# Optimization experiments

Hardware: AMD Instinct MI355X
Metric: run time of the kernel (lower is better)

The kernel has to match this reference:

```python
import jax, jax.numpy as jnp
import numpy as np
import math

B, S, H, D = 4, 2048, 16, 64
HID = H * D  # 1024


def setup_inputs() -> dict:
    key = jax.random.key(0)
    ks = jax.random.split(key, 9)
    s_in = 1.0 / math.sqrt(D)
    s_hid = 1.0 / math.sqrt(HID)
    return {
        "x": jax.random.normal(ks[0], (B, S, D), dtype=jnp.float32),
        "Wq": jax.random.uniform(ks[1], (D, HID), jnp.float32, -s_in, s_in),
        "bq": jax.random.uniform(ks[2], (HID,), jnp.float32, -s_in, s_in),
        "Wk": jax.random.uniform(ks[3], (D, HID), jnp.float32, -s_in, s_in),
        "bk": jax.random.uniform(ks[4], (HID,), jnp.float32, -s_in, s_in),
        "Wv": jax.random.uniform(ks[5], (D, HID), jnp.float32, -s_in, s_in),
        "bv": jax.random.uniform(ks[6], (HID,), jnp.float32, -s_in, s_in),
        "Wo": jax.random.uniform(ks[7], (HID, D), jnp.float32, -s_hid, s_hid),
        "bo": jax.random.uniform(ks[8], (D,), jnp.float32, -s_hid, s_hid),
    }


def reference(x, Wq, bq, Wk, bk, Wv, bv, Wo, bo):
    b, s, _ = x.shape
    # projections: [B,S,D] -> [B,S,HID] -> [B,H,S,D]
    q = (x @ Wq + bq).reshape(b, s, H, D).transpose(0, 2, 1, 3)
    k = (x @ Wk + bk).reshape(b, s, H, D).transpose(0, 2, 1, 3)
    v = (x @ Wv + bv).reshape(b, s, H, D).transpose(0, 2, 1, 3)
    scores = jnp.einsum("bhqd,bhkd->bhqk", q, k) / math.sqrt(D)
    # causal mask: -inf strictly above the diagonal
    causal = jnp.tril(jnp.ones((s, s), dtype=bool))
    scores = jnp.where(causal, scores, -jnp.inf)
    attn = jax.nn.softmax(scores, axis=-1)  # dropout is identity at eval
    out = jnp.einsum("bhqk,bhkd->bhqd", attn, v)
    out = out.transpose(0, 2, 1, 3).reshape(b, s, HID)
    return out @ Wo + bo  # [B,S,D]
```

## Files before the change

### kernel.cpp

```cpp
#include <hip/hip_runtime.h>
#include <hip/hip_bf16.h>

#define B 4
#define S 2048
#define H 16
#define D 64
#define HID 1024

typedef __hip_bfloat16 bf16;
typedef __attribute__((ext_vector_type(8))) short bf16x8;
typedef __attribute__((ext_vector_type(4))) short bf16x4;
typedef __attribute__((ext_vector_type(4))) float f32x4;

static __device__ __forceinline__ float b2f(bf16 v) { return __bfloat162float(v); }

static __device__ __forceinline__ unsigned pkbf(float a, float b) {
    union { bf16 h; unsigned short u; } ua, ub;
    ua.h = __float2bfloat16(a);
    ub.h = __float2bfloat16(b);
    return (unsigned)ua.u | ((unsigned)ub.u << 16);
}

#define SCL 0.18033688011112042f

#define QSTR 72
#define VTS  132

__global__ __launch_bounds__(256) void qkv_mfma_kernel(
    const float* __restrict__ x,
    const float* __restrict__ Wq, const float* __restrict__ bq,
    const float* __restrict__ Wk, const float* __restrict__ bk,
    const float* __restrict__ Wv, const float* __restrict__ bv,
    bf16* __restrict__ q, bf16* __restrict__ k, bf16* __restrict__ v)
{
    __shared__ __align__(16) char smem[36864];
    __shared__ float bs[128];
    bf16* Xs = (bf16*)smem;
    bf16* Wt = (bf16*)(smem + 128 * QSTR * 2);

    const int tid = threadIdx.x;
    const int mat = blockIdx.y >> 3;
    const int N0  = (blockIdx.y & 7) * 128;
    const int m0  = blockIdx.x * 128;

    const float* W    = (mat == 0) ? Wq : (mat == 1) ? Wk : Wv;
    const float* bias = (mat == 0) ? bq : (mat == 1) ? bk : bv;
    bf16*        dst  = (mat == 0) ? q  : (mat == 1) ? k  : v;
    const float  oscale = (mat == 0) ? SCL : 1.0f;

    #pragma unroll
    for (int i = 0; i < 8; ++i) {
        int item = i * 256 + tid;
        int row = item >> 4, f4 = item & 15;
        float4 xv = *(const float4*)&x[(size_t)(m0 + row) * D + f4 * 4];
        union { bf16 h[4]; bf16x4 v4; } u;
        u.h[0] = __float2bfloat16(xv.x); u.h[1] = __float2bfloat16(xv.y);
        u.h[2] = __float2bfloat16(xv.z); u.h[3] = __float2bfloat16(xv.w);
        *(bf16x4*)&Xs[row * QSTR + f4 * 4] = u.v4;
    }
    #pragma unroll
    for (int i = 0; i < 2; ++i) {
        int unit = i * 256 + tid;
        int n0 = (unit & 31) * 4, k0 = (unit >> 5) * 4;
        float wv[4][4];
        #pragma unroll
        for (int j = 0; j < 4; ++j) {
            float4 t = *(const float4*)&W[(size_t)(k0 + j) * HID + N0 + n0];
            wv[j][0] = t.x; wv[j][1] = t.y; wv[j][2] = t.z; wv[j][3] = t.w;
        }
        #pragma unroll
        for (int dn = 0; dn < 4; ++dn) {
            union { bf16 h[4]; bf16x4 v4; } u;
            #pragma unroll
            for (int j = 0; j < 4; ++j) u.h[j] = __float2bfloat16(wv[j][dn]);
            *(bf16x4*)&Wt[(n0 + dn) * QSTR + k0] = u.v4;
        }
    }
    if (tid < 128) bs[tid] = bias[N0 + tid];
    __syncthreads();

    const int lane = tid & 63, wave = tid >> 6;
    const int c = lane & 15, quad = lane >> 4;

    bf16x8 af[2][2];
    #pragma unroll
    for (int mg = 0; mg < 2; ++mg)
        #pragma unroll
        for (int kc = 0; kc < 2; ++kc)
            af[mg][kc] = *(const bf16x8*)&Xs[(wave * 32 + mg * 16 + c) * QSTR + kc * 32 + quad * 8];

    f32x4 acc[2][8];
    #pragma unroll
    for (int mg = 0; mg < 2; ++mg)
        #pragma unroll
        for (int ng = 0; ng < 8; ++ng)
            acc[mg][ng] = (f32x4){0.f, 0.f, 0.f, 0.f};

    if (mat == 2) {
        #pragma unroll
        for (int ng = 0; ng < 8; ++ng) {
            bf16x8 bf0 = *(const bf16x8*)&Wt[(ng * 16 + c) * QSTR + quad * 8];
            bf16x8 bf1 = *(const bf16x8*)&Wt[(ng * 16 + c) * QSTR + 32 + quad * 8];
            #pragma unroll
            for (int mg = 0; mg < 2; ++mg) {
                acc[mg][ng] = __builtin_amdgcn_mfma_f32_16x16x32_bf16(af[mg][0], bf0, acc[mg][ng], 0, 0, 0);
                acc[mg][ng] = __builtin_amdgcn_mfma_f32_16x16x32_bf16(af[mg][1], bf1, acc[mg][ng], 0, 0, 0);
            }
        }
    } else {
        #pragma unroll
        for (int ng = 0; ng < 8; ++ng) {
            bf16x8 bf0 = *(const bf16x8*)&Wt[(ng * 16 + c) * QSTR + quad * 8];
            bf16x8 bf1 = *(const bf16x8*)&Wt[(ng * 16 + c) * QSTR + 32 + quad * 8];
            #pragma unroll
            for (int mg = 0; mg < 2; ++mg) {
                acc[mg][ng] = __builtin_amdgcn_mfma_f32_16x16x32_bf16(bf0, af[mg][0], acc[mg][ng], 0, 0, 0);
                acc[mg][ng] = __builtin_amdgcn_mfma_f32_16x16x32_bf16(bf1, af[mg][1], acc[mg][ng], 0, 0, 0);
            }
        }
    }

    if (mat == 2) {
        bf16* T = (bf16*)smem;
        __syncthreads();
        #pragma unroll
        for (int ng = 0; ng < 8; ++ng) {
            int hid_l = ng * 16 + c;
            float bb_ = bs[hid_l];
            #pragma unroll
            for (int mg = 0; mg < 2; ++mg) {
                int ss_l = wave * 32 + mg * 16 + quad * 4;
                union { bf16 h4[4]; bf16x4 v4; } u;
                #pragma unroll
                for (int r = 0; r < 4; ++r)
                    u.h4[r] = __float2bfloat16(acc[mg][ng][r] + bb_);
                *(bf16x4*)&T[hid_l * VTS + ss_l] = u.v4;
            }
        }
        __syncthreads();
        const int b_ = m0 >> 11, ss0 = m0 & (S - 1);
        #pragma unroll
        for (int pass = 0; pass < 8; ++pass) {
            int unit = pass * 256 + tid;
            int dd_l = unit >> 4, u8 = unit & 15;
            bf16x8 val = *(const bf16x8*)&T[dd_l * VTS + u8 * 8];
            int h = (N0 >> 6) + (dd_l >> 6), ddg = dd_l & 63;
            *(bf16x8*)&dst[((size_t)(b_ * H + h) * D + ddg) * S + ss0 + u8 * 8] = val;
        }
    } else {
        bf16* T2 = (bf16*)smem;
        __syncthreads();
        #pragma unroll
        for (int ng = 0; ng < 8; ++ng) {
            float4 bb4 = *(const float4*)&bs[ng * 16 + quad * 4];
            #pragma unroll
            for (int mg = 0; mg < 2; ++mg) {
                int mrow = wave * 32 + mg * 16 + c;
                union { bf16 h4[4]; bf16x4 v4; } u;
                #pragma unroll
                for (int r = 0; r < 4; ++r)
                    u.h4[r] = __float2bfloat16((acc[mg][ng][r] + (&bb4.x)[r]) * oscale);
                *(bf16x4*)&T2[mrow * VTS + ng * 16 + quad * 4] = u.v4;
            }
        }
        __syncthreads();
        const int b_ = m0 >> 11, ss0 = m0 & (S - 1);
        #pragma unroll
        for (int pass = 0; pass < 8; ++pass) {
            int unit = pass * 256 + tid;
            int row_l = unit >> 4, n8 = unit & 15;
            bf16x8 val = *(const bf16x8*)&T2[row_l * VTS + n8 * 8];
            int n_g = N0 + n8 * 8;
            int h = n_g >> 6, dd = n_g & 63;
            *(bf16x8*)&dst[((size_t)(b_ * H + h) * S + ss0 + row_l) * D + dd] = val;
        }
    }
}

#define BT   64
#define NT   (S / BT)

__global__ __launch_bounds__(256) void flash_mfma_kernel(
    const bf16* __restrict__ qg, const bf16* __restrict__ kg,
    const bf16* __restrict__ vg, bf16* __restrict__ og)
{
    __shared__ bf16 Ks[2][BT * 64];
    __shared__ bf16 Vt[2][BT * 64];
    __shared__ bf16 Ps[4][16 * 64];

    const int tid  = threadIdx.x;
    const int wave = tid >> 6;
    const int lane = tid & 63;
    const int c    = lane & 15;
    const int quad = lane >> 4;

    const int L    = (int)blockIdx.x + 16 * (int)blockIdx.y;
    const int xcd  = L & 7;
    const int slot = L >> 3;
    const int pair = slot & 15;
    const int bh   = xcd * 8 + (slot >> 4);
    const int b_   = bh >> 4, h_ = bh & 15;
    const size_t hbase = (size_t)bh * S * D;
    bf16* myP = &Ps[wave][0];
    const int srow = wave * 16 + c;

    const int qta = pair;
    const int qtb = NT - 1 - pair;

    const int sr0 = tid >> 3, g0 = tid & 7;
    const int sr1 = sr0 + 32;
    const int sc0 = g0 * 8;
    const int so0 = sr0 * 64 + ((g0 ^ (sr0 & 7)) << 3);
    const int so1 = sr1 * 64 + ((g0 ^ (sr1 & 7)) << 3);
    const int cx7 = c & 7;

    bf16x8 qfa0, qfa1, qfb0, qfb1;
    {
        const size_t ra = hbase + (size_t)(qta * BT + srow) * D;
        const size_t rb = hbase + (size_t)(qtb * BT + srow) * D;
        qfa0 = *(const bf16x8*)(qg + ra + quad * 8);
        qfa1 = *(const bf16x8*)(qg + ra + 32 + quad * 8);
        qfb0 = *(const bf16x8*)(qg + rb + quad * 8);
        qfb1 = *(const bf16x8*)(qg + rb + 32 + quad * 8);
    }

    float la = 0.f, lb = 0.f;
    f32x4 ota[4], otb[4];
    #pragma unroll
    for (int jn = 0; jn < 4; ++jn) {
        ota[jn] = (f32x4){0.f, 0.f, 0.f, 0.f};
        otb[jn] = (f32x4){0.f, 0.f, 0.f, 0.f};
    }

    auto front = [&](const bf16* Kb, bf16x8 qf0, bf16x8 qf1, float& l1, bool diag) {
        f32x4 st[4];
        #pragma unroll
        for (int jn = 0; jn < 4; ++jn) {
            const int rb_ = (jn * 16 + c) * 64;
            bf16x8 kf0 = *(const bf16x8*)&Kb[rb_ + ((quad       ^ cx7) << 3)];
            bf16x8 kf1 = *(const bf16x8*)&Kb[rb_ + (((quad + 4) ^ cx7) << 3)];
            f32x4 s = {0.f, 0.f, 0.f, 0.f};
            s = __builtin_amdgcn_mfma_f32_16x16x32_bf16(kf0, qf0, s, 0, 0, 0);
            s = __builtin_amdgcn_mfma_f32_16x16x32_bf16(kf1, qf1, s, 0, 0, 0);
            st[jn] = s;
        }
        #pragma unroll
        for (int jn = 0; jn < 4; ++jn) {
            float p0 = __builtin_amdgcn_exp2f(st[jn][0]);
            float p1 = __builtin_amdgcn_exp2f(st[jn][1]);
            float p2 = __builtin_amdgcn_exp2f(st[jn][2]);
            float p3 = __builtin_amdgcn_exp2f(st[jn][3]);
            if (diag) {
                int col = jn * 16 + quad * 4;
                if (col     > srow) p0 = 0.f;
                if (col + 1 > srow) p1 = 0.f;
                if (col + 2 > srow) p2 = 0.f;
                if (col + 3 > srow) p3 = 0.f;
            }
            l1 += (p0 + p1) + (p2 + p3);
            union { unsigned w[2]; bf16x4 v4; } pk;
            pk.w[0] = pkbf(p0, p1);
            pk.w[1] = pkbf(p2, p3);
            *(bf16x4*)&myP[c * 64 + (((2 * jn + (quad >> 1)) ^ cx7) << 3) + (quad & 1) * 4] = pk.v4;
        }
    };
    auto pv = [&](const bf16* Vb, f32x4* ot) {
        #pragma unroll
        for (int kc = 0; kc < 2; ++kc) {
            bf16x8 pf = *(const bf16x8*)&myP[c * 64 + (((kc * 4 + quad) ^ cx7) << 3)];
            #pragma unroll
            for (int jn = 0; jn < 4; ++jn) {
                const int rb_ = (jn * 16 + c) * 64;
                bf16x8 vf = *(const bf16x8*)&Vb[rb_ + (((kc * 4 + quad) ^ cx7) << 3)];
                ot[jn] = __builtin_amdgcn_mfma_f32_16x16x32_bf16(vf, pf, ot[jn], 0, 0, 0);
            }
        }
    };

    bf16x8 kreg0, kreg1, vreg0, vreg1;
    kreg0 = *(const bf16x8*)(kg + hbase + (size_t)sr0 * D + sc0);
    kreg1 = *(const bf16x8*)(kg + hbase + (size_t)sr1 * D + sc0);
    vreg0 = *(const bf16x8*)(vg + hbase + (size_t)sr0 * S + sc0);
    vreg1 = *(const bf16x8*)(vg + hbase + (size_t)sr1 * S + sc0);
    *(bf16x8*)&Ks[0][so0] = kreg0;
    *(bf16x8*)&Ks[0][so1] = kreg1;
    *(bf16x8*)&Vt[0][so0] = vreg0;
    *(bf16x8*)&Vt[0][so1] = vreg1;
    {
        const int nb = BT;
        kreg0 = *(const bf16x8*)(kg + hbase + (size_t)(nb + sr0) * D + sc0);
        kreg1 = *(const bf16x8*)(kg + hbase + (size_t)(nb + sr1) * D + sc0);
        vreg0 = *(const bf16x8*)(vg + hbase + (size_t)sr0 * S + nb + sc0);
        vreg1 = *(const bf16x8*)(vg + hbase + (size_t)sr1 * S + nb + sc0);
    }
    __syncthreads();

    int cur = 0;
    for (int kt = 0; kt <= qtb; ++kt) {
        if (kt < qtb) {
            *(bf16x8*)&Ks[cur ^ 1][so0] = kreg0;
            *(bf16x8*)&Ks[cur ^ 1][so1] = kreg1;
            *(bf16x8*)&Vt[cur ^ 1][so0] = vreg0;
            *(bf16x8*)&Vt[cur ^ 1][so1] = vreg1;
            if (kt + 1 < qtb) {
                const int nb = (kt + 2) * BT;
                kreg0 = *(const bf16x8*)(kg + hbase + (size_t)(nb + sr0) * D + sc0);
                kreg1 = *(const bf16x8*)(kg + hbase + (size_t)(nb + sr1) * D + sc0);
                vreg0 = *(const bf16x8*)(vg + hbase + (size_t)sr0 * S + nb + sc0);
                vreg1 = *(const bf16x8*)(vg + hbase + (size_t)sr1 * S + nb + sc0);
            }
        }

        const bf16* Kb = &Ks[cur][0];
        const bf16* Vb = &Vt[cur][0];
        front(Kb, qfb0, qfb1, lb, kt == qtb);
        pv(Vb, otb);
        if (kt <= qta) {
            front(Kb, qfa0, qfa1, la, kt == qta);
            pv(Vb, ota);
        }

        if (kt < qtb) {
            __syncthreads();
            cur ^= 1;
        }
    }

    {
        float lt = lb;
        lt += __shfl_xor(lt, 16);
        lt += __shfl_xor(lt, 32);
        const float inv = 1.f / lt;
        const size_t obase = ((size_t)(b_ * S + qtb * BT + srow)) * HID + h_ * 64 + quad * 4;
        #pragma unroll
        for (int jn = 0; jn < 4; ++jn) {
            union { bf16 h4[4]; bf16x4 v4; } u;
            #pragma unroll
            for (int r = 0; r < 4; ++r)
                u.h4[r] = __float2bfloat16(otb[jn][r] * inv);
            *(bf16x4*)&og[obase + jn * 16] = u.v4;
        }
    }
    {
        float lt = la;
        lt += __shfl_xor(lt, 16);
        lt += __shfl_xor(lt, 32);
        const float inv = 1.f / lt;
        const size_t obase = ((size_t)(b_ * S + qta * BT + srow)) * HID + h_ * 64 + quad * 4;
        #pragma unroll
        for (int jn = 0; jn < 4; ++jn) {
            union { bf16 h4[4]; bf16x4 v4; } u;
            #pragma unroll
            for (int r = 0; r < 4; ++r)
                u.h4[r] = __float2bfloat16(ota[jn][r] * inv);
            *(bf16x4*)&og[obase + jn * 16] = u.v4;
        }
    }
}

__global__ __launch_bounds__(256) void out_proj_mfma_kernel(
    const bf16* __restrict__ o, const float* __restrict__ Wo,
    const float* __restrict__ bo, float* __restrict__ out)
{
    __shared__ bf16 Os[32 * QSTR];
    __shared__ bf16 Wot[64 * QSTR];
    __shared__ float bos[64];

    const int tid = threadIdx.x;
    const int m0  = blockIdx.x * 32;
    const int lane = tid & 63, wave = tid >> 6;
    const int c = lane & 15, quad = lane >> 4;
    const int mtile = wave >> 1;
    const int ngb   = (wave & 1) * 2;

    const int orow = tid >> 3, ooct = tid & 7;
    const int n0 = (tid & 15) * 4, kk0 = (tid >> 4) * 4;

    if (tid < 64) bos[tid] = bo[tid];

    bf16x8 oreg = *(const bf16x8*)(o + (size_t)(m0 + orow) * HID + ooct * 8);
    float4 w4[4];
    #pragma unroll
    for (int j = 0; j < 4; ++j)
        w4[j] = *(const float4*)&Wo[(size_t)(kk0 + j) * 64 + n0];

    f32x4 acc[2];
    acc[0] = (f32x4){0.f, 0.f, 0.f, 0.f};
    acc[1] = (f32x4){0.f, 0.f, 0.f, 0.f};

    for (int chunk = 0; chunk < 16; ++chunk) {
        __syncthreads();
        *(bf16x8*)&Os[orow * QSTR + ooct * 8] = oreg;
        #pragma unroll
        for (int dn = 0; dn < 4; ++dn) {
            union { bf16 h[4]; bf16x4 v4; } u;
            u.h[0] = __float2bfloat16((&w4[0].x)[dn]);
            u.h[1] = __float2bfloat16((&w4[1].x)[dn]);
            u.h[2] = __float2bfloat16((&w4[2].x)[dn]);
            u.h[3] = __float2bfloat16((&w4[3].x)[dn]);
            *(bf16x4*)&Wot[(n0 + dn) * QSTR + kk0] = u.v4;
        }
        __syncthreads();

        if (chunk < 15) {
            const int k1 = (chunk + 1) * 64;
            oreg = *(const bf16x8*)(o + (size_t)(m0 + orow) * HID + k1 + ooct * 8);
            #pragma unroll
            for (int j = 0; j < 4; ++j)
                w4[j] = *(const float4*)&Wo[(size_t)(k1 + kk0 + j) * 64 + n0];
        }

        bf16x8 a0 = *(const bf16x8*)&Os[(mtile * 16 + c) * QSTR + quad * 8];
        bf16x8 a1 = *(const bf16x8*)&Os[(mtile * 16 + c) * QSTR + 32 + quad * 8];
        #pragma unroll
        for (int g = 0; g < 2; ++g) {
            int ng = ngb + g;
            bf16x8 b0 = *(const bf16x8*)&Wot[(ng * 16 + c) * QSTR + quad * 8];
            bf16x8 b1 = *(const bf16x8*)&Wot[(ng * 16 + c) * QSTR + 32 + quad * 8];
            acc[g] = __builtin_amdgcn_mfma_f32_16x16x32_bf16(a0, b0, acc[g], 0, 0, 0);
            acc[g] = __builtin_amdgcn_mfma_f32_16x16x32_bf16(a1, b1, acc[g], 0, 0, 0);
        }
    }

    #pragma unroll
    for (int g = 0; g < 2; ++g) {
        int n = (ngb + g) * 16 + c;
        float bb_ = bos[n];
        #pragma unroll
        for (int r = 0; r < 4; ++r) {
            int row = m0 + mtile * 16 + quad * 4 + r;
            out[(size_t)row * 64 + n] = acc[g][r] + bb_;
        }
    }
}

extern "C" void kernel_launch(void* const* d_in, const int* in_sizes, int n_in,
                              void* d_out, int out_size, void* d_ws, size_t ws_size,
                              hipStream_t stream)
{
    const float* x  = (const float*)d_in[0];
    const float* Wq = (const float*)d_in[1];
    const float* bq = (const float*)d_in[2];
    const float* Wk = (const float*)d_in[3];
    const float* bk = (const float*)d_in[4];
    const float* Wv = (const float*)d_in[5];
    const float* bv = (const float*)d_in[6];
    const float* Wo = (const float*)d_in[7];
    const float* bo = (const float*)d_in[8];

    char* ws = (char*)d_ws;
    const size_t qkv_bytes = (size_t)B * S * HID * sizeof(bf16);
    bf16* qw = (bf16*)(ws);
    bf16* kw = (bf16*)(ws + qkv_bytes);
    bf16* vw = (bf16*)(ws + 2 * qkv_bytes);
    bf16* ow = (bf16*)(ws + 3 * qkv_bytes);

    qkv_mfma_kernel<<<dim3(B * S / 128, 24), 256, 0, stream>>>(
        x, Wq, bq, Wk, bk, Wv, bv, qw, kw, vw);

    flash_mfma_kernel<<<dim3(NT / 2, B * H), 256, 0, stream>>>(qw, kw, vw, ow);

    out_proj_mfma_kernel<<<dim3(B * S / 32), 256, 0, stream>>>(ow, Wo, bo,
                                                               (float*)d_out);
}
```

Before: 162.9 us.

## Fuse Q/K/V projections into one block loop reusing x fragments in registers

The QKV kernel now launches 8 column blocks instead of 24, and each block loops over the three weight matrices. The x tile is loaded once straight from global memory into MFMA A-fragments in registers, with no LDS staging, and reused for Q, K and V. This cuts redundant x loads and conversions but gives a third as many blocks with longer serial work each. The flash kernel also gains explicit lgkmcnt waits between the P writes and the PV reads, and packs P through a uint2 store.

```diff
diff --git a/kernel.cpp b/kernel.cpp
--- a/kernel.cpp
+++ b/kernel.cpp
@@ -35,144 +35,145 @@
 {
     __shared__ __align__(16) char smem[36864];
     __shared__ float bs[128];
-    bf16* Xs = (bf16*)smem;
-    bf16* Wt = (bf16*)(smem + 128 * QSTR * 2);
+    bf16* Wt = (bf16*)smem;
 
     const int tid = threadIdx.x;
-    const int mat = blockIdx.y >> 3;
-    const int N0  = (blockIdx.y & 7) * 128;
+    const int N0  = blockIdx.y * 128;
     const int m0  = blockIdx.x * 128;
-
-    const float* W    = (mat == 0) ? Wq : (mat == 1) ? Wk : Wv;
-    const float* bias = (mat == 0) ? bq : (mat == 1) ? bk : bv;
-    bf16*        dst  = (mat == 0) ? q  : (mat == 1) ? k  : v;
-    const float  oscale = (mat == 0) ? SCL : 1.0f;
-
-    #pragma unroll
-    for (int i = 0; i < 8; ++i) {
-        int item = i * 256 + tid;
-        int row = item >> 4, f4 = item & 15;
-        float4 xv = *(const float4*)&x[(size_t)(m0 + row) * D + f4 * 4];
-        union { bf16 h[4]; bf16x4 v4; } u;
-        u.h[0] = __float2bfloat16(xv.x); u.h[1] = __float2bfloat16(xv.y);
-        u.h[2] = __float2bfloat16(xv.z); u.h[3] = __float2bfloat16(xv.w);
-        *(bf16x4*)&Xs[row * QSTR + f4 * 4] = u.v4;
-    }
-    #pragma unroll
-    for (int i = 0; i < 2; ++i) {
-        int unit = i * 256 + tid;
-        int n0 = (unit & 31) * 4, k0 = (unit >> 5) * 4;
-        float wv[4][4];
-        #pragma unroll
-        for (int j = 0; j < 4; ++j) {
-            float4 t = *(const float4*)&W[(size_t)(k0 + j) * HID + N0 + n0];
-            wv[j][0] = t.x; wv[j][1] = t.y; wv[j][2] = t.z; wv[j][3] = t.w;
-        }
-        #pragma unroll
-        for (int dn = 0; dn < 4; ++dn) {
-            union { bf16 h[4]; bf16x4 v4; } u;
-            #pragma unroll
-            for (int j = 0; j < 4; ++j) u.h[j] = __float2bfloat16(wv[j][dn]);
-            *(bf16x4*)&Wt[(n0 + dn) * QSTR + k0] = u.v4;
-        }
-    }
-    if (tid < 128) bs[tid] = bias[N0 + tid];
-    __syncthreads();
 
     const int lane = tid & 63, wave = tid >> 6;
     const int c = lane & 15, quad = lane >> 4;
 
     bf16x8 af[2][2];
     #pragma unroll
-    for (int mg = 0; mg < 2; ++mg)
-        #pragma unroll
-        for (int kc = 0; kc < 2; ++kc)
-            af[mg][kc] = *(const bf16x8*)&Xs[(wave * 32 + mg * 16 + c) * QSTR + kc * 32 + quad * 8];
-
-    f32x4 acc[2][8];
-    #pragma unroll
-    for (int mg = 0; mg < 2; ++mg)
-        #pragma unroll
-        for (int ng = 0; ng < 8; ++ng)
-            acc[mg][ng] = (f32x4){0.f, 0.f, 0.f, 0.f};
-
-    if (mat == 2) {
-        #pragma unroll
-        for (int ng = 0; ng < 8; ++ng) {
-            bf16x8 bf0 = *(const bf16x8*)&Wt[(ng * 16 + c) * QSTR + quad * 8];
-            bf16x8 bf1 = *(const bf16x8*)&Wt[(ng * 16 + c) * QSTR + 32 + quad * 8];
-            #pragma unroll
-            for (int mg = 0; mg < 2; ++mg) {
-                acc[mg][ng] = __builtin_amdgcn_mfma_f32_16x16x32_bf16(af[mg][0], bf0, acc[mg][ng], 0, 0, 0);
-                acc[mg][ng] = __builtin_amdgcn_mfma_f32_16x16x32_bf16(af[mg][1], bf1, acc[mg][ng], 0, 0, 0);
-            }
-        }
-    } else {
-        #pragma unroll
-        for (int ng = 0; ng < 8; ++ng) {
-            bf16x8 bf0 = *(const bf16x8*)&Wt[(ng * 16 + c) * QSTR + quad * 8];
-            bf16x8 bf1 = *(const bf16x8*)&Wt[(ng * 16 + c) * QSTR + 32 + quad * 8];
-            #pragma unroll
-            for (int mg = 0; mg < 2; ++mg) {
-                acc[mg][ng] = __builtin_amdgcn_mfma_f32_16x16x32_bf16(bf0, af[mg][0], acc[mg][ng], 0, 0, 0);
-                acc[mg][ng] = __builtin_amdgcn_mfma_f32_16x16x32_bf16(bf1, af[mg][1], acc[mg][ng], 0, 0, 0);
-            }
-        }
-    }
-
-    if (mat == 2) {
-        bf16* T = (bf16*)smem;
+    for (int mg = 0; mg < 2; ++mg) {
+        const float* xr = &x[(size_t)(m0 + wave * 32 + mg * 16 + c) * D];
+        #pragma unroll
+        for (int kc = 0; kc < 2; ++kc) {
+            float4 lo = *(const float4*)&xr[kc * 32 + quad * 8];
+            float4 hi = *(const float4*)&xr[kc * 32 + quad * 8 + 4];
+            union { bf16 h[8]; bf16x8 v8; } u;
+            u.h[0] = __float2bfloat16(lo.x); u.h[1] = __float2bfloat16(lo.y);
+            u.h[2] = __float2bfloat16(lo.z); u.h[3] = __float2bfloat16(lo.w);
+            u.h[4] = __float2bfloat16(hi.x); u.h[5] = __float2bfloat16(hi.y);
+            u.h[6] = __float2bfloat16(hi.z); u.h[7] = __float2bfloat16(hi.w);
+            af[mg][kc] = u.v8;
+        }
+    }
+
+    const int b_ = m0 >> 11, ss0 = m0 & (S - 1);
+
+    for (int mat = 0; mat < 3; ++mat) {
+        const float* W    = (mat == 0) ? Wq : (mat == 1) ? Wk : Wv;
+        const float* bias = (mat == 0) ? bq : (mat == 1) ? bk : bv;
+        bf16*        dst  = (mat == 0) ? q  : (mat == 1) ? k  : v;
+        const float  oscale = (mat == 0) ? SCL : 1.0f;
+
         __syncthreads();
         #pragma unroll
-        for (int ng = 0; ng < 8; ++ng) {
-            int hid_l = ng * 16 + c;
-            float bb_ = bs[hid_l];
-            #pragma unroll
-            for (int mg = 0; mg < 2; ++mg) {
-                int ss_l = wave * 32 + mg * 16 + quad * 4;
-                union { bf16 h4[4]; bf16x4 v4; } u;
+        for (int i = 0; i < 2; ++i) {
+            int unit = i * 256 + tid;
+            int n0 = (unit & 31) * 4, k0 = (unit >> 5) * 4;
+            float wv[4][4];
+            #pragma unroll
+            for (int j = 0; j < 4; ++j) {
+                float4 t = *(const float4*)&W[(size_t)(k0 + j) * HID + N0 + n0];
+                wv[j][0] = t.x; wv[j][1] = t.y; wv[j][2] = t.z; wv[j][3] = t.w;
+            }
+            #pragma unroll
+            for (int dn = 0; dn < 4; ++dn) {
+                union { bf16 h[4]; bf16x4 v4; } u;
                 #pragma unroll
-                for (int r = 0; r < 4; ++r)
-                    u.h4[r] = __float2bfloat16(acc[mg][ng][r] + bb_);
-                *(bf16x4*)&T[hid_l * VTS + ss_l] = u.v4;
-            }
-        }
+                for (int j = 0; j < 4; ++j) u.h[j] = __float2bfloat16(wv[j][dn]);
+                *(bf16x4*)&Wt[(n0 + dn) * QSTR + k0] = u.v4;
+            }
+        }
+        if (tid < 128) bs[tid] = bias[N0 + tid];
         __syncthreads();
-        const int b_ = m0 >> 11, ss0 = m0 & (S - 1);
-        #pragma unroll
-        for (int pass = 0; pass < 8; ++pass) {
-            int unit = pass * 256 + tid;
-            int dd_l = unit >> 4, u8 = unit & 15;
-            bf16x8 val = *(const bf16x8*)&T[dd_l * VTS + u8 * 8];
-            int h = (N0 >> 6) + (dd_l >> 6), ddg = dd_l & 63;
-            *(bf16x8*)&dst[((size_t)(b_ * H + h) * D + ddg) * S + ss0 + u8 * 8] = val;
-        }
-    } else {
-        bf16* T2 = (bf16*)smem;
+
+        f32x4 acc[2][8];
+        #pragma unroll
+        for (int mg = 0; mg < 2; ++mg)
+            #pragma unroll
+            for (int ng = 0; ng < 8; ++ng)
+                acc[mg][ng] = (f32x4){0.f, 0.f, 0.f, 0.f};
+
+        if (mat == 2) {
+            #pragma unroll
+            for (int ng = 0; ng < 8; ++ng) {
+                bf16x8 bf0 = *(const bf16x8*)&Wt[(ng * 16 + c) * QSTR + quad * 8];
+                bf16x8 bf1 = *(const bf16x8*)&Wt[(ng * 16 + c) * QSTR + 32 + quad * 8];
+                #pragma unroll
+                for (int mg = 0; mg < 2; ++mg) {
+                    acc[mg][ng] = __builtin_amdgcn_mfma_f32_16x16x32_bf16(af[mg][0], bf0, acc[mg][ng], 0, 0, 0);
+                    acc[mg][ng] = __builtin_amdgcn_mfma_f32_16x16x32_bf16(af[mg][1], bf1, acc[mg][ng], 0, 0, 0);
+                }
+            }
+        } else {
+            #pragma unroll
+            for (int ng = 0; ng < 8; ++ng) {
+                bf16x8 bf0 = *(const bf16x8*)&Wt[(ng * 16 + c) * QSTR + quad * 8];
+                bf16x8 bf1 = *(const bf16x8*)&Wt[(ng * 16 + c) * QSTR + 32 + quad * 8];
+                #pragma unroll
+                for (int mg = 0; mg < 2; ++mg) {
+                    acc[mg][ng] = __builtin_amdgcn_mfma_f32_16x16x32_bf16(bf0, af[mg][0], acc[mg][ng], 0, 0, 0);
+                    acc[mg][ng] = __builtin_amdgcn_mfma_f32_16x16x32_bf16(bf1, af[mg][1], acc[mg][ng], 0, 0, 0);
+                }
+            }
+        }
+
         __syncthreads();
-        #pragma unroll
-        for (int ng = 0; ng < 8; ++ng) {
-            float4 bb4 = *(const float4*)&bs[ng * 16 + quad * 4];
-            #pragma unroll
-            for (int mg = 0; mg < 2; ++mg) {
-                int mrow = wave * 32 + mg * 16 + c;
-                union { bf16 h4[4]; bf16x4 v4; } u;
+
+        if (mat == 2) {
+            bf16* T = (bf16*)smem;
+            #pragma unroll
+            for (int ng = 0; ng < 8; ++ng) {
+                int hid_l = ng * 16 + c;
+                float bb_ = bs[hid_l];
                 #pragma unroll
-                for (int r = 0; r < 4; ++r)
-                    u.h4[r] = __float2bfloat16((acc[mg][ng][r] + (&bb4.x)[r]) * oscale);
-                *(bf16x4*)&T2[mrow * VTS + ng * 16 + quad * 4] = u.v4;
-            }
-        }
-        __syncthreads();
-        const int b_ = m0 >> 11, ss0 = m0 & (S - 1);
-        #pragma unroll
-        for (int pass = 0; pass < 8; ++pass) {
-            int unit = pass * 256 + tid;
-            int row_l = unit >> 4, n8 = unit & 15;
-            bf16x8 val = *(const bf16x8*)&T2[row_l * VTS + n8 * 8];
-            int n_g = N0 + n8 * 8;
-            int h = n_g >> 6, dd = n_g & 63;
-            *(bf16x8*)&dst[((size_t)(b_ * H + h) * S + ss0 + row_l) * D + dd] = val;
+                for (int mg = 0; mg < 2; ++mg) {
+                    int ss_l = wave * 32 + mg * 16 + quad * 4;
+                    union { bf16 h4[4]; bf16x4 v4; } u;
+                    #pragma unroll
+                    for (int r = 0; r < 4; ++r)
+                        u.h4[r] = __float2bfloat16(acc[mg][ng][r] + bb_);
+                    *(bf16x4*)&T[hid_l * VTS + ss_l] = u.v4;
+                }
+            }
+            __syncthreads();
+            #pragma unroll
+            for (int pass = 0; pass < 8; ++pass) {
+                int unit = pass * 256 + tid;
+                int dd_l = unit >> 4, u8 = unit & 15;
+                bf16x8 val = *(const bf16x8*)&T[dd_l * VTS + u8 * 8];
+                int h = (N0 >> 6) + (dd_l >> 6), ddg = dd_l & 63;
+                *(bf16x8*)&dst[((size_t)(b_ * H + h) * D + ddg) * S + ss0 + u8 * 8] = val;
+            }
+        } else {
+            bf16* T2 = (bf16*)smem;
+            #pragma unroll
+            for (int ng = 0; ng < 8; ++ng) {
+                float4 bb4 = *(const float4*)&bs[ng * 16 + quad * 4];
+                #pragma unroll
+                for (int mg = 0; mg < 2; ++mg) {
+                    int mrow = wave * 32 + mg * 16 + c;
+                    union { bf16 h4[4]; bf16x4 v4; } u;
+                    #pragma unroll
+                    for (int r = 0; r < 4; ++r)
+                        u.h4[r] = __float2bfloat16((acc[mg][ng][r] + (&bb4.x)[r]) * oscale);
+                    *(bf16x4*)&T2[mrow * VTS + ng * 16 + quad * 4] = u.v4;
+                }
+            }
+            __syncthreads();
+            #pragma unroll
+            for (int pass = 0; pass < 8; ++pass) {
+                int unit = pass * 256 + tid;
+                int row_l = unit >> 4, n8 = unit & 15;
+                bf16x8 val = *(const bf16x8*)&T2[row_l * VTS + n8 * 8];
+                int n_g = N0 + n8 * 8;
+                int h = n_g >> 6, dd = n_g & 63;
+                *(bf16x8*)&dst[((size_t)(b_ * H + h) * S + ss0 + row_l) * D + dd] = val;
+            }
         }
     }
 }
@@ -258,10 +259,10 @@
                 if (col + 3 > srow) p3 = 0.f;
             }
             l1 += (p0 + p1) + (p2 + p3);
-            union { unsigned w[2]; bf16x4 v4; } pk;
-            pk.w[0] = pkbf(p0, p1);
-            pk.w[1] = pkbf(p2, p3);
-            *(bf16x4*)&myP[c * 64 + (((2 * jn + (quad >> 1)) ^ cx7) << 3) + (quad & 1) * 4] = pk.v4;
+            uint2 pk;
+            pk.x = pkbf(p0, p1);
+            pk.y = pkbf(p2, p3);
+            *(uint2*)&myP[c * 64 + (((2 * jn + (quad >> 1)) ^ cx7) << 3) + (quad & 1) * 4] = pk;
         }
     };
     auto pv = [&](const bf16* Vb, f32x4* ot) {
@@ -314,9 +315,11 @@
         const bf16* Kb = &Ks[cur][0];
         const bf16* Vb = &Vt[cur][0];
         front(Kb, qfb0, qfb1, lb, kt == qtb);
+        asm volatile("s_waitcnt lgkmcnt(0)" ::: "memory");
         pv(Vb, otb);
         if (kt <= qta) {
             front(Kb, qfa0, qfa1, la, kt == qta);
+            asm volatile("s_waitcnt lgkmcnt(0)" ::: "memory");
             pv(Vb, ota);
         }
 
@@ -455,7 +458,7 @@
     bf16* vw = (bf16*)(ws + 2 * qkv_bytes);
     bf16* ow = (bf16*)(ws + 3 * qkv_bytes);
 
-    qkv_mfma_kernel<<<dim3(B * S / 128, 24), 256, 0, stream>>>(
+    qkv_mfma_kernel<<<dim3(B * S / 128, 8), 256, 0, stream>>>(
         x, Wq, bq, Wk, bk, Wv, bv, qw, kw, vw);
 
     flash_mfma_kernel<<<dim3(NT / 2, B * H), 256, 0, stream>>>(qw, kw, vw, ow);
```

New measurement: 165.6 us. No clear change (+1.7%).

## Double-buffer out-projection LDS tiles and add LDS waitcnt before PV in attention

Applied to the files above, without the earlier changes.

The out-projection kernel now uses two LDS buffers for the O and Wo tiles. The next chunk is staged while the current one is consumed, so each iteration needs one barrier instead of two. The attention loop adds an explicit s_waitcnt lgkmcnt(0) between writing P to LDS and reading it back in the PV step, which may fix or strengthen ordering of the per-wave P buffer. The P packing also switches from a union to a uint2 store. Double buffering doubles the out-projection LDS use, and the explicit waits may reduce the compiler's freedom to overlap.

```diff
diff --git a/kernel.cpp b/kernel.cpp
--- a/kernel.cpp
+++ b/kernel.cpp
@@ -258,10 +258,10 @@
                 if (col + 3 > srow) p3 = 0.f;
             }
             l1 += (p0 + p1) + (p2 + p3);
-            union { unsigned w[2]; bf16x4 v4; } pk;
-            pk.w[0] = pkbf(p0, p1);
-            pk.w[1] = pkbf(p2, p3);
-            *(bf16x4*)&myP[c * 64 + (((2 * jn + (quad >> 1)) ^ cx7) << 3) + (quad & 1) * 4] = pk.v4;
+            uint2 pk;
+            pk.x = pkbf(p0, p1);
+            pk.y = pkbf(p2, p3);
+            *(uint2*)&myP[c * 64 + (((2 * jn + (quad >> 1)) ^ cx7) << 3) + (quad & 1) * 4] = pk;
         }
     };
     auto pv = [&](const bf16* Vb, f32x4* ot) {
@@ -314,9 +314,11 @@
         const bf16* Kb = &Ks[cur][0];
         const bf16* Vb = &Vt[cur][0];
         front(Kb, qfb0, qfb1, lb, kt == qtb);
+        asm volatile("s_waitcnt lgkmcnt(0)" ::: "memory");
         pv(Vb, otb);
         if (kt <= qta) {
             front(Kb, qfa0, qfa1, la, kt == qta);
+            asm volatile("s_waitcnt lgkmcnt(0)" ::: "memory");
             pv(Vb, ota);
         }
 
@@ -362,8 +364,8 @@
     const bf16* __restrict__ o, const float* __restrict__ Wo,
     const float* __restrict__ bo, float* __restrict__ out)
 {
-    __shared__ bf16 Os[32 * QSTR];
-    __shared__ bf16 Wot[64 * QSTR];
+    __shared__ bf16 Os[2][32 * QSTR];
+    __shared__ bf16 Wot[2][64 * QSTR];
     __shared__ float bos[64];
 
     const int tid = threadIdx.x;
@@ -384,13 +386,8 @@
     for (int j = 0; j < 4; ++j)
         w4[j] = *(const float4*)&Wo[(size_t)(kk0 + j) * 64 + n0];
 
-    f32x4 acc[2];
-    acc[0] = (f32x4){0.f, 0.f, 0.f, 0.f};
-    acc[1] = (f32x4){0.f, 0.f, 0.f, 0.f};
-
-    for (int chunk = 0; chunk < 16; ++chunk) {
-        __syncthreads();
-        *(bf16x8*)&Os[orow * QSTR + ooct * 8] = oreg;
+    auto stage = [&](int buf) {
+        *(bf16x8*)&Os[buf][orow * QSTR + ooct * 8] = oreg;
         #pragma unroll
         for (int dn = 0; dn < 4; ++dn) {
             union { bf16 h[4]; bf16x4 v4; } u;
@@ -398,27 +395,51 @@
             u.h[1] = __float2bfloat16((&w4[1].x)[dn]);
             u.h[2] = __float2bfloat16((&w4[2].x)[dn]);
             u.h[3] = __float2bfloat16((&w4[3].x)[dn]);
-            *(bf16x4*)&Wot[(n0 + dn) * QSTR + kk0] = u.v4;
-        }
-        __syncthreads();
-
+            *(bf16x4*)&Wot[buf][(n0 + dn) * QSTR + kk0] = u.v4;
+        }
+    };
+
+    stage(0);
+    {
+        const int k1 = 64;
+        oreg = *(const bf16x8*)(o + (size_t)(m0 + orow) * HID + k1 + ooct * 8);
+        #pragma unroll
+        for (int j = 0; j < 4; ++j)
+            w4[j] = *(const float4*)&Wo[(size_t)(k1 + kk0 + j) * 64 + n0];
+    }
+    __syncthreads();
+
+    f32x4 acc[2];
+    acc[0] = (f32x4){0.f, 0.f, 0.f, 0.f};
+    acc[1] = (f32x4){0.f, 0.f, 0.f, 0.f};
+
+    int cur = 0;
+    for (int chunk = 0; chunk < 16; ++chunk) {
         if (chunk < 15) {
-            const int k1 = (chunk + 1) * 64;
-            oreg = *(const bf16x8*)(o + (size_t)(m0 + orow) * HID + k1 + ooct * 8);
-            #pragma unroll
-            for (int j = 0; j < 4; ++j)
-                w4[j] = *(const float4*)&Wo[(size_t)(k1 + kk0 + j) * 64 + n0];
-        }
-
-        bf16x8 a0 = *(const bf16x8*)&Os[(mtile * 16 + c) * QSTR + quad * 8];
-        bf16x8 a1 = *(const bf16x8*)&Os[(mtile * 16 + c) * QSTR + 32 + quad * 8];
+            stage(cur ^ 1);
+            if (chunk + 1 < 15) {
+                const int k2 = (chunk + 2) * 64;
+                oreg = *(const bf16x8*)(o + (size_t)(m0 + orow) * HID + k2 + ooct * 8);
+                #pragma unroll
+                for (int j = 0; j < 4; ++j)
+                    w4[j] = *(const float4*)&Wo[(size_t)(k2 + kk0 + j) * 64 + n0];
+            }
+        }
+
+        bf16x8 a0 = *(const bf16x8*)&Os[cur][(mtile * 16 + c) * QSTR + quad * 8];
+        bf16x8 a1 = *(const bf16x8*)&Os[cur][(mtile * 16 + c) * QSTR + 32 + quad * 8];
         #pragma unroll
         for (int g = 0; g < 2; ++g) {
             int ng = ngb + g;
-            bf16x8 b0 = *(const bf16x8*)&Wot[(ng * 16 + c) * QSTR + quad * 8];
-            bf16x8 b1 = *(const bf16x8*)&Wot[(ng * 16 + c) * QSTR + 32 + quad * 8];
+            bf16x8 b0 = *(const bf16x8*)&Wot[cur][(ng * 16 + c) * QSTR + quad * 8];
+            bf16x8 b1 = *(const bf16x8*)&Wot[cur][(ng * 16 + c) * QSTR + 32 + quad * 8];
             acc[g] = __builtin_amdgcn_mfma_f32_16x16x32_bf16(a0, b0, acc[g], 0, 0, 0);
             acc[g] = __builtin_amdgcn_mfma_f32_16x16x32_bf16(a1, b1, acc[g], 0, 0, 0);
+        }
+
+        if (chunk < 15) {
+            __syncthreads();
+            cur ^= 1;
         }
     }
 
```

New measurement: 160.0 us. About the same (-1.7%).
